# Optimization experiments

Hardware: AMD Instinct MI355X
Metric: run time of the kernel (lower is better)

## Reference

```python
import jax, jax.numpy as jnp
import numpy as np

ALPHA = 0.1      # LeakyReLU negative slope from GAT.__init__
NEG_INF = -9e15  # standard pyGAT masking constant


def gat_layer(x, adj, W, a_src, a_dst):
    """Single-head GraphAttentionLayer (n_heads=1, concat=True, dropout=0)."""
    Wh = x @ W                              # [N, F]
    f_src = Wh @ a_src                      # [N]
    f_dst = Wh @ a_dst                      # [N]
    e = jax.nn.leaky_relu(f_src[:, None] + f_dst[None, :], negative_slope=ALPHA)  # [N, N]
    e = jnp.where(adj > 0, e, NEG_INF)
    attn = jax.nn.softmax(e, axis=1)        # row-wise segment softmax over neighbors
    out = attn @ Wh                         # [N, F]
    return jax.nn.relu(out)                 # activate_function = 'relu'


def setup_inputs() -> dict:
    key = jax.random.key(0)
    ks = jax.random.split(key, 8)
    N, D_IN, D_HID, D_OUT = 8192, 256, 200, 128
    A_hat = (jax.random.uniform(ks[0], (N, N)) < 0.005).astype(jnp.float32)
    x = jax.random.normal(ks[1], (N, D_IN), dtype=jnp.float32)
    W1 = jax.random.normal(ks[2], (D_IN, D_HID), dtype=jnp.float32) * (1.0 / np.sqrt(D_IN))
    a1_src = jax.random.normal(ks[3], (D_HID,), dtype=jnp.float32) * 0.1
    a1_dst = jax.random.normal(ks[4], (D_HID,), dtype=jnp.float32) * 0.1
    W2 = jax.random.normal(ks[5], (D_HID, D_OUT), dtype=jnp.float32) * (1.0 / np.sqrt(D_HID))
    a2_src = jax.random.normal(ks[6], (D_OUT,), dtype=jnp.float32) * 0.1
    a2_dst = jax.random.normal(ks[7], (D_OUT,), dtype=jnp.float32) * 0.1
    return {"A_hat": A_hat, "x": x, "W1": W1, "a1_src": a1_src, "a1_dst": a1_dst,
            "W2": W2, "a2_src": a2_src, "a2_dst": a2_dst}


def reference(A_hat, x, W1, a1_src, a1_dst, W2, a2_src, a2_dst):
    # forward_direct with num_GCN_blocks = 2 (directed graph: A and A^T branches)
    A_t = A_hat.T
    params = [(W1, a1_src, a1_dst), (W2, a2_src, a2_dst)]
    outputs = [x]
    h1, h2 = x, x
    for (W, asrc, adst) in params:
        o1 = gat_layer(h1, A_hat, W, asrc, adst)
        o2 = gat_layer(h2, A_t, W, asrc, adst)
        outputs.append(jnp.concatenate([o1, o2], axis=1))
        h1, h2 = o1, o2
    return tuple(outputs)
```

## Files before the change

kernel.cpp:

```cpp
#include <hip/hip_runtime.h>
#include <hip/hip_bf16.h>

#define NN 8192
#define CAP 128
#define ALPHA 0.1f

typedef __attribute__((ext_vector_type(8))) short bf16x8;
typedef __attribute__((ext_vector_type(4))) float f32x4;
typedef __attribute__((ext_vector_type(4))) float nfloat4;

__global__ __launch_bounds__(256) void build_ell_rows(
        const float* __restrict__ A, int* __restrict__ deg,
        int* __restrict__ ell, int* __restrict__ degT,
        int* __restrict__ ellT) {
    __shared__ int cnt;
    __shared__ int idxs[CAP];
    const int i = blockIdx.x;
    const int tid = threadIdx.x;
    if (tid == 0) cnt = 0;
    __syncthreads();
    const nfloat4* rowA = (const nfloat4*)(A + (size_t)i * NN);
#pragma unroll
    for (int it = 0; it < NN / 4 / 256; ++it) {
        nfloat4 v = __builtin_nontemporal_load(&rowA[it * 256 + tid]);
        int j0 = (it * 256 + tid) * 4;
#pragma unroll
        for (int u = 0; u < 4; ++u) {
            if (v[u] > 0.f) {
                int p = atomicAdd(&cnt, 1);
                if (p < CAP) idxs[p] = j0 + u;
            }
        }
    }
    __syncthreads();
    int c = cnt;
    if (tid == 0) deg[i] = c;
    if (c > CAP) c = CAP;
    for (int t = tid; t < c; t += 256) {
        int j = idxs[t];
        ell[i * CAP + t] = j;
        int q = atomicAdd(&degT[j], 1);
        if (q < CAP) ellT[j * CAP + q] = i;
    }
}

__global__ void conv_bf16(const float* __restrict__ src,
                          __hip_bfloat16* __restrict__ dst, long long n) {
    long long i = ((long long)blockIdx.x * blockDim.x + threadIdx.x) * 4;
    if (i + 3 < n) {
        float4 v = *(const float4*)(src + i);
        dst[i + 0] = __float2bfloat16(v.x);
        dst[i + 1] = __float2bfloat16(v.y);
        dst[i + 2] = __float2bfloat16(v.z);
        dst[i + 3] = __float2bfloat16(v.w);
    } else {
        for (; i < n; ++i) dst[i] = __float2bfloat16(src[i]);
    }
}

__global__ void prep_wt(const float* __restrict__ W, int K, int N,
                        __hip_bfloat16* __restrict__ WT, int Kpad, int Npad) {
    int idx = blockIdx.x * blockDim.x + threadIdx.x;
    if (idx >= Npad * Kpad) return;
    int n = idx / Kpad, k = idx % Kpad;
    float v = (n < N && k < K) ? W[(size_t)k * N + n] : 0.f;
    WT[idx] = __float2bfloat16(v);
}

__global__ __launch_bounds__(256) void gemm_mfma(
        const __hip_bfloat16* __restrict__ Ab, int lda, long long aBatch,
        const __hip_bfloat16* __restrict__ BTb, int ldb,
        float* __restrict__ C, int ldc, long long cBatch,
        int Kpad, int Ncols) {
    __shared__ __hip_bfloat16 As[64 * 32];
    __shared__ __hip_bfloat16 Bs[64 * 32];
    const int tid = threadIdx.x;
    const int wave = tid >> 6, lane = tid & 63;
    const int bm = blockIdx.y * 64, bn = blockIdx.x * 64;
    const __hip_bfloat16* Abz = Ab + (size_t)blockIdx.z * aBatch;
    float* Cz = C + (size_t)blockIdx.z * cBatch;

    const int sr = tid >> 2, sc = tid & 3;
    const int kh_a = sc ^ ((sr >> 1) & 3);
    const __hip_bfloat16* gA = Abz + (size_t)(bm + sr) * lda + kh_a * 8;
    const __hip_bfloat16* gB = BTb + (size_t)(bn + sr) * ldb + kh_a * 8;
    char* ldsA = (char*)As + wave * 1024;
    char* ldsB = (char*)Bs + wave * 1024;

    const int fr = lane & 15;
    const int kh = lane >> 4;
    const int ar = wave * 16 + fr;
    const int aoff = ar * 64 + ((kh ^ ((ar >> 1) & 3)) * 16);
    int boff[4];
#pragma unroll
    for (int cb = 0; cb < 4; ++cb) {
        int bc = cb * 16 + fr;
        boff[cb] = bc * 64 + ((kh ^ ((bc >> 1) & 3)) * 16);
    }

    f32x4 acc[4] = {};
    for (int k0 = 0; k0 < Kpad; k0 += 32) {
        __builtin_amdgcn_global_load_lds(
            (const __attribute__((address_space(1))) void*)(gA + k0),
            (__attribute__((address_space(3))) void*)ldsA, 16, 0, 0);
        __builtin_amdgcn_global_load_lds(
            (const __attribute__((address_space(1))) void*)(gB + k0),
            (__attribute__((address_space(3))) void*)ldsB, 16, 0, 0);
        asm volatile("s_waitcnt vmcnt(0)" ::: "memory");
        __syncthreads();
        bf16x8 afrag = *(const bf16x8*)((const char*)As + aoff);
#pragma unroll
        for (int cb = 0; cb < 4; ++cb) {
            bf16x8 bfrag = *(const bf16x8*)((const char*)Bs + boff[cb]);
            acc[cb] = __builtin_amdgcn_mfma_f32_16x16x32_bf16(afrag, bfrag,
                                                              acc[cb], 0, 0, 0);
        }
        __syncthreads();
    }
    const int crow = bm + wave * 16 + (lane >> 4) * 4;
#pragma unroll
    for (int cb = 0; cb < 4; ++cb) {
        int col = bn + cb * 16 + (lane & 15);
        if (col < Ncols) {
#pragma unroll
            for (int r = 0; r < 4; ++r)
                Cz[(size_t)(crow + r) * ldc + col] = acc[cb][r];
        }
    }
}

__global__ void fvec_kernel(const float* __restrict__ Wh, int ldw, int F,
                            const float* __restrict__ asrc,
                            const float* __restrict__ adst,
                            float* __restrict__ fs, float* __restrict__ fd,
                            int M) {
    int wave = (int)((blockIdx.x * (long long)blockDim.x + threadIdx.x) >> 6);
    int lane = threadIdx.x & 63;
    if (wave >= M) return;
    const float* row = Wh + (long long)wave * ldw;
    float s = 0.f, d = 0.f;
    for (int k = lane; k < F; k += 64) {
        float w = row[k];
        s += w * asrc[k];
        d += w * adst[k];
    }
#pragma unroll
    for (int off = 32; off > 0; off >>= 1) {
        s += __shfl_down(s, off);
        d += __shfl_down(d, off);
    }
    if (lane == 0) { fs[wave] = s; fd[wave] = d; }
}

__global__ __launch_bounds__(128) void attn_kernel(
        const int* __restrict__ ell, const int* __restrict__ deg,
        const int* __restrict__ ellT, const int* __restrict__ degT,
        const float* __restrict__ fs, const float* __restrict__ fd,
        long long fStride,
        const float* __restrict__ Wh, long long whStride, int ldw, int F,
        float* __restrict__ out, int ldo,
        __hip_bfloat16* __restrict__ hb, long long hbStride, int ldh) {
    __shared__ float p[CAP];
    __shared__ int nbr[CAP];
    __shared__ float red[2];
    const int i = blockIdx.x;
    const int br = blockIdx.y;
    const int tid = threadIdx.x;
    const int* ep = br ? ellT : ell;
    const int* dp = br ? degT : deg;
    const float* fsp = fs + (size_t)br * fStride;
    const float* fdp = fd + (size_t)br * fStride;
    const float* Whp = Wh + (size_t)br * whStride;
    float* outp = out + br * F;
    __hip_bfloat16* hbp = hb ? hb + (size_t)br * hbStride : nullptr;

    int d = dp[i];
    if (d > CAP) d = CAP;

    if (d == 0) {
        for (int f = tid; f < F; f += blockDim.x) {
            float acc = 0.f;
            for (int j = 0; j < NN; ++j) acc += Whp[(long long)j * ldw + f];
            float v = acc / (float)NN;
            v = v > 0.f ? v : 0.f;
            outp[(long long)i * ldo + f] = v;
            if (hbp) hbp[(long long)i * ldh + f] = __float2bfloat16(v);
        }
        if (hbp)
            for (int f = F + tid; f < ldh; f += blockDim.x)
                hbp[(long long)i * ldh + f] = __float2bfloat16(0.f);
        return;
    }

    float fsi = fsp[i];
    if (tid < d) {
        int j = ep[i * CAP + tid];
        nbr[tid] = j;
        float e = fsi + fdp[j];
        p[tid] = e > 0.f ? e : ALPHA * e;
    }
    __syncthreads();
    if (tid < 64) {
        float m = -1e30f;
        for (int t = tid; t < d; t += 64) m = fmaxf(m, p[t]);
#pragma unroll
        for (int off = 32; off > 0; off >>= 1) m = fmaxf(m, __shfl_down(m, off));
        if (tid == 0) red[0] = m;
    }
    __syncthreads();
    float m = red[0];
    if (tid < d) p[tid] = __expf(p[tid] - m);
    __syncthreads();
    if (tid < 64) {
        float s = 0.f;
        for (int t = tid; t < d; t += 64) s += p[t];
#pragma unroll
        for (int off = 32; off > 0; off >>= 1) s += __shfl_down(s, off);
        if (tid == 0) red[1] = s;
    }
    __syncthreads();
    if (tid < d) p[tid] *= (1.f / red[1]);
    __syncthreads();

    const int fh = F >> 1;
    if (tid < fh) {
        float ax = 0.f, ay = 0.f;
        int t = 0;
        for (; t + 4 <= d; t += 4) {
            float2 w0 = ((const float2*)(Whp + (long long)nbr[t + 0] * ldw))[tid];
            float2 w1 = ((const float2*)(Whp + (long long)nbr[t + 1] * ldw))[tid];
            float2 w2 = ((const float2*)(Whp + (long long)nbr[t + 2] * ldw))[tid];
            float2 w3 = ((const float2*)(Whp + (long long)nbr[t + 3] * ldw))[tid];
            ax += p[t] * w0.x + p[t + 1] * w1.x + p[t + 2] * w2.x + p[t + 3] * w3.x;
            ay += p[t] * w0.y + p[t + 1] * w1.y + p[t + 2] * w2.y + p[t + 3] * w3.y;
        }
        for (; t < d; ++t) {
            float2 w = ((const float2*)(Whp + (long long)nbr[t] * ldw))[tid];
            ax += p[t] * w.x;
            ay += p[t] * w.y;
        }
        ax = ax > 0.f ? ax : 0.f;
        ay = ay > 0.f ? ay : 0.f;
        float2 v2 = {ax, ay};
        *(float2*)(outp + (long long)i * ldo + 2 * tid) = v2;
        if (hbp) {
            hbp[(long long)i * ldh + 2 * tid]     = __float2bfloat16(ax);
            hbp[(long long)i * ldh + 2 * tid + 1] = __float2bfloat16(ay);
        }
    } else if (hbp && 2 * tid < ldh) {
        hbp[(long long)i * ldh + 2 * tid]     = __float2bfloat16(0.f);
        hbp[(long long)i * ldh + 2 * tid + 1] = __float2bfloat16(0.f);
    }
}

static inline char* carve(char*& w, size_t bytes) {
    char* p = w;
    w += (bytes + 255) & ~(size_t)255;
    return p;
}

extern "C" void kernel_launch(void* const* d_in, const int* in_sizes, int n_in,
                              void* d_out, int out_size, void* d_ws,
                              size_t ws_size, hipStream_t stream) {
    const float* A   = (const float*)d_in[0];
    const float* x   = (const float*)d_in[1];
    const float* W1  = (const float*)d_in[2];
    const float* a1s = (const float*)d_in[3];
    const float* a1d = (const float*)d_in[4];
    const float* W2  = (const float*)d_in[5];
    const float* a2s = (const float*)d_in[6];
    const float* a2d = (const float*)d_in[7];
    float* out = (float*)d_out;

    const int D_IN = 256, D_HID = 200, D_OUT = 128;
    const int KP1 = 256;
    const int HP  = 224;
    const int NP1 = 256;

    char* w = (char*)d_ws;
    int* deg  = (int*)carve(w, NN * 4);
    int* degT = (int*)carve(w, NN * 4);
    int* ell  = (int*)carve(w, (size_t)NN * CAP * 4);
    int* ellT = (int*)carve(w, (size_t)NN * CAP * 4);
    float* Wh1 = (float*)carve(w, (size_t)NN * D_HID * 4);
    float* Wh2 = (float*)carve(w, (size_t)2 * NN * D_OUT * 4);
    float* fs1 = (float*)carve(w, NN * 4);
    float* fd1 = (float*)carve(w, NN * 4);
    float* fs2 = (float*)carve(w, (size_t)2 * NN * 4);
    float* fd2 = (float*)carve(w, (size_t)2 * NN * 4);
    __hip_bfloat16* xb   = (__hip_bfloat16*)carve(w, (size_t)NN * KP1 * 2);
    __hip_bfloat16* W1Tb = (__hip_bfloat16*)carve(w, (size_t)NP1 * KP1 * 2);
    __hip_bfloat16* W2Tb = (__hip_bfloat16*)carve(w, (size_t)D_OUT * HP * 2);
    __hip_bfloat16* h1b  = (__hip_bfloat16*)carve(w, (size_t)2 * NN * HP * 2);

    float* out0 = out;
    float* out1 = out + (size_t)NN * D_IN;
    float* out2 = out1 + (size_t)NN * 2 * D_HID;

    (void)hipMemsetAsync(degT, 0, NN * 4, stream);
    (void)hipMemcpyAsync(out0, x, (size_t)NN * D_IN * 4,
                         hipMemcpyDeviceToDevice, stream);

    conv_bf16<<<(NN * D_IN / 4 + 255) / 256, 256, 0, stream>>>(
        x, xb, (long long)NN * D_IN);
    prep_wt<<<(NP1 * KP1 + 255) / 256, 256, 0, stream>>>(W1, D_IN, D_HID,
                                                         W1Tb, KP1, NP1);
    prep_wt<<<(D_OUT * HP + 255) / 256, 256, 0, stream>>>(W2, D_HID, D_OUT,
                                                          W2Tb, HP, D_OUT);
    build_ell_rows<<<NN, 256, 0, stream>>>(A, deg, ell, degT, ellT);

    gemm_mfma<<<dim3(4, NN / 64, 1), 256, 0, stream>>>(
        xb, KP1, 0, W1Tb, KP1, Wh1, D_HID, 0, KP1, D_HID);
    fvec_kernel<<<NN / 4, 256, 0, stream>>>(Wh1, D_HID, D_HID, a1s, a1d, fs1,
                                            fd1, NN);
    attn_kernel<<<dim3(NN, 2), 128, 0, stream>>>(
        ell, deg, ellT, degT, fs1, fd1, 0, Wh1, 0, D_HID, D_HID,
        out1, 2 * D_HID, h1b, (long long)NN * HP, HP);

    gemm_mfma<<<dim3(2, NN / 64, 2), 256, 0, stream>>>(
        h1b, HP, (long long)NN * HP, W2Tb, HP, Wh2, D_OUT,
        (long long)NN * D_OUT, HP, D_OUT);
    fvec_kernel<<<2 * NN / 4, 256, 0, stream>>>(Wh2, D_OUT, D_OUT, a2s, a2d,
                                                fs2, fd2, 2 * NN);
    attn_kernel<<<dim3(NN, 2), 128, 0, stream>>>(
        ell, deg, ellT, degT, fs2, fd2, (long long)NN,
        Wh2, (long long)NN * D_OUT, D_OUT, D_OUT,
        out2, 2 * D_OUT, nullptr, 0, 0);
}
```

Before: 484.0 us.

## Fuse prep kernels, GEMM with attention-vector epilogue, and use single-wave attention

The code merges the x copy, bf16 conversions, weight transposes and buffer zeroing into one prep kernel, and runs the first GEMM and the ELL build in the same launch. The f_src/f_dst dot products move into the GEMM epilogue as atomic adds, which removes the separate fvec kernels. Attention now uses one 64-lane wave per row with float4 loads, shuffle-based softmax and no LDS barriers. The goal is fewer launches and less synchronisation overhead. In exchange, atomic accumulation makes the fs/fd summation order nondeterministic.

```diff
diff --git a/kernel.cpp b/kernel.cpp
--- a/kernel.cpp
+++ b/kernel.cpp
@@ -9,86 +9,66 @@
 typedef __attribute__((ext_vector_type(4))) float f32x4;
 typedef __attribute__((ext_vector_type(4))) float nfloat4;
 
-__global__ __launch_bounds__(256) void build_ell_rows(
-        const float* __restrict__ A, int* __restrict__ deg,
-        int* __restrict__ ell, int* __restrict__ degT,
-        int* __restrict__ ellT) {
-    __shared__ int cnt;
-    __shared__ int idxs[CAP];
-    const int i = blockIdx.x;
-    const int tid = threadIdx.x;
-    if (tid == 0) cnt = 0;
-    __syncthreads();
-    const nfloat4* rowA = (const nfloat4*)(A + (size_t)i * NN);
-#pragma unroll
-    for (int it = 0; it < NN / 4 / 256; ++it) {
-        nfloat4 v = __builtin_nontemporal_load(&rowA[it * 256 + tid]);
-        int j0 = (it * 256 + tid) * 4;
-#pragma unroll
-        for (int u = 0; u < 4; ++u) {
-            if (v[u] > 0.f) {
-                int p = atomicAdd(&cnt, 1);
-                if (p < CAP) idxs[p] = j0 + u;
-            }
-        }
-    }
-    __syncthreads();
-    int c = cnt;
-    if (tid == 0) deg[i] = c;
-    if (c > CAP) c = CAP;
-    for (int t = tid; t < c; t += 256) {
-        int j = idxs[t];
-        ell[i * CAP + t] = j;
-        int q = atomicAdd(&degT[j], 1);
-        if (q < CAP) ellT[j * CAP + q] = i;
-    }
-}
-
-__global__ void conv_bf16(const float* __restrict__ src,
-                          __hip_bfloat16* __restrict__ dst, long long n) {
-    long long i = ((long long)blockIdx.x * blockDim.x + threadIdx.x) * 4;
-    if (i + 3 < n) {
-        float4 v = *(const float4*)(src + i);
-        dst[i + 0] = __float2bfloat16(v.x);
-        dst[i + 1] = __float2bfloat16(v.y);
-        dst[i + 2] = __float2bfloat16(v.z);
-        dst[i + 3] = __float2bfloat16(v.w);
+static __device__ __forceinline__ unsigned short f2bf(float f) {
+    __hip_bfloat16 b = __float2bfloat16(f);
+    return *reinterpret_cast<unsigned short*>(&b);
+}
+
+__global__ __launch_bounds__(256) void prep_all(
+        const float* __restrict__ x, const float* __restrict__ W1,
+        const float* __restrict__ W2, __hip_bfloat16* __restrict__ xb,
+        __hip_bfloat16* __restrict__ W1Tb, __hip_bfloat16* __restrict__ W2Tb,
+        float* __restrict__ out0, int* __restrict__ degT,
+        float* __restrict__ fzero) {
+    const int b = blockIdx.x, tid = threadIdx.x;
+    if (b < 2048) {
+        long long i = ((long long)b * 256 + tid) * 4;
+        nfloat4 v = *(const nfloat4*)(x + i);
+        *(nfloat4*)(out0 + i) = v;
+        ushort4 h;
+        h.x = f2bf(v[0]); h.y = f2bf(v[1]); h.z = f2bf(v[2]); h.w = f2bf(v[3]);
+        *(ushort4*)(xb + i) = h;
+    } else if (b < 2104) {
+        int wb = b - 2048;
+        int w0 = wb * 1024 + tid * 4;
+        if (w0 < 8192) {
+            int4 z = {0, 0, 0, 0};
+            *(int4*)(degT + w0) = z;
+        } else {
+            nfloat4 z = {0.f, 0.f, 0.f, 0.f};
+            *(nfloat4*)(fzero + (w0 - 8192)) = z;
+        }
+    } else if (b < 2360) {
+        int idx = (b - 2104) * 256 + tid;
+        int n = idx >> 8, k = idx & 255;
+        W1Tb[idx] = __float2bfloat16(n < 200 ? W1[(size_t)k * 200 + n] : 0.f);
     } else {
-        for (; i < n; ++i) dst[i] = __float2bfloat16(src[i]);
-    }
-}
-
-__global__ void prep_wt(const float* __restrict__ W, int K, int N,
-                        __hip_bfloat16* __restrict__ WT, int Kpad, int Npad) {
-    int idx = blockIdx.x * blockDim.x + threadIdx.x;
-    if (idx >= Npad * Kpad) return;
-    int n = idx / Kpad, k = idx % Kpad;
-    float v = (n < N && k < K) ? W[(size_t)k * N + n] : 0.f;
-    WT[idx] = __float2bfloat16(v);
-}
-
-__global__ __launch_bounds__(256) void gemm_mfma(
-        const __hip_bfloat16* __restrict__ Ab, int lda, long long aBatch,
+        int idx = (b - 2360) * 256 + tid;
+        int n = idx / 224, k = idx % 224;
+        W2Tb[idx] = __float2bfloat16(k < 200 ? W2[(size_t)k * 128 + n] : 0.f);
+    }
+}
+
+__device__ __forceinline__ void gemm_body(
+        char* smem, int bm, int bn,
+        const __hip_bfloat16* __restrict__ Ab, int lda,
         const __hip_bfloat16* __restrict__ BTb, int ldb,
-        float* __restrict__ C, int ldc, long long cBatch,
-        int Kpad, int Ncols) {
-    __shared__ __hip_bfloat16 As[64 * 32];
-    __shared__ __hip_bfloat16 Bs[64 * 32];
+        float* __restrict__ C, int ldc, int Kpad, int Ncols,
+        const float* __restrict__ asrc, const float* __restrict__ adst,
+        float* __restrict__ fs, float* __restrict__ fd) {
+    __hip_bfloat16* As = (__hip_bfloat16*)smem;
+    __hip_bfloat16* Bs = (__hip_bfloat16*)(smem + 4096);
     const int tid = threadIdx.x;
     const int wave = tid >> 6, lane = tid & 63;
-    const int bm = blockIdx.y * 64, bn = blockIdx.x * 64;
-    const __hip_bfloat16* Abz = Ab + (size_t)blockIdx.z * aBatch;
-    float* Cz = C + (size_t)blockIdx.z * cBatch;
 
     const int sr = tid >> 2, sc = tid & 3;
     const int kh_a = sc ^ ((sr >> 1) & 3);
-    const __hip_bfloat16* gA = Abz + (size_t)(bm + sr) * lda + kh_a * 8;
+    const __hip_bfloat16* gA = Ab + (size_t)(bm + sr) * lda + kh_a * 8;
     const __hip_bfloat16* gB = BTb + (size_t)(bn + sr) * ldb + kh_a * 8;
     char* ldsA = (char*)As + wave * 1024;
     char* ldsB = (char*)Bs + wave * 1024;
 
-    const int fr = lane & 15;
-    const int kh = lane >> 4;
+    const int fr = lane & 15, kh = lane >> 4;
     const int ar = wave * 16 + fr;
     const int aoff = ar * 64 + ((kh ^ ((ar >> 1) & 3)) * 16);
     int boff[4];
@@ -117,139 +97,210 @@
         }
         __syncthreads();
     }
-    const int crow = bm + wave * 16 + (lane >> 4) * 4;
+
+    const int crow = bm + wave * 16 + kh * 4;
+    float as4[4], ad4[4];
+    int cols[4];
 #pragma unroll
     for (int cb = 0; cb < 4; ++cb) {
-        int col = bn + cb * 16 + (lane & 15);
+        int col = bn + cb * 16 + fr;
+        cols[cb] = col;
+        bool v = col < Ncols;
+        as4[cb] = v ? asrc[col] : 0.f;
+        ad4[cb] = v ? adst[col] : 0.f;
+    }
+#pragma unroll
+    for (int r = 0; r < 4; ++r) {
+        float s = 0.f, dd = 0.f;
+#pragma unroll
+        for (int cb = 0; cb < 4; ++cb) {
+            s += acc[cb][r] * as4[cb];
+            dd += acc[cb][r] * ad4[cb];
+        }
+#pragma unroll
+        for (int off = 8; off > 0; off >>= 1) {
+            s += __shfl_down(s, off, 16);
+            dd += __shfl_down(dd, off, 16);
+        }
+        if (fr == 0) {
+            atomicAdd(&fs[crow + r], s);
+            atomicAdd(&fd[crow + r], dd);
+        }
+    }
+#pragma unroll
+    for (int cb = 0; cb < 4; ++cb) {
+        int col = cols[cb];
         if (col < Ncols) {
 #pragma unroll
             for (int r = 0; r < 4; ++r)
-                Cz[(size_t)(crow + r) * ldc + col] = acc[cb][r];
-        }
-    }
-}
-
-__global__ void fvec_kernel(const float* __restrict__ Wh, int ldw, int F,
-                            const float* __restrict__ asrc,
-                            const float* __restrict__ adst,
-                            float* __restrict__ fs, float* __restrict__ fd,
-                            int M) {
-    int wave = (int)((blockIdx.x * (long long)blockDim.x + threadIdx.x) >> 6);
-    int lane = threadIdx.x & 63;
-    if (wave >= M) return;
-    const float* row = Wh + (long long)wave * ldw;
-    float s = 0.f, d = 0.f;
-    for (int k = lane; k < F; k += 64) {
-        float w = row[k];
-        s += w * asrc[k];
-        d += w * adst[k];
-    }
-#pragma unroll
-    for (int off = 32; off > 0; off >>= 1) {
-        s += __shfl_down(s, off);
-        d += __shfl_down(d, off);
-    }
-    if (lane == 0) { fs[wave] = s; fd[wave] = d; }
-}
-
-__global__ __launch_bounds__(128) void attn_kernel(
+                C[(size_t)(crow + r) * ldc + col] = acc[cb][r];
+        }
+    }
+}
+
+__global__ __launch_bounds__(256) void mega1(
+        const __hip_bfloat16* __restrict__ xb,
+        const __hip_bfloat16* __restrict__ W1Tb, float* __restrict__ Wh1,
+        const float* __restrict__ a1s, const float* __restrict__ a1d,
+        float* __restrict__ fs1, float* __restrict__ fd1,
+        const float* __restrict__ A, int* __restrict__ deg,
+        int* __restrict__ ell, int* __restrict__ degT,
+        int* __restrict__ ellT) {
+    __shared__ __align__(16) char smem[8192];
+    if (blockIdx.x < 512) {
+        gemm_body(smem, (int)(blockIdx.x >> 2) * 64, (int)(blockIdx.x & 3) * 64,
+                  xb, 256, W1Tb, 256, Wh1, 200, 256, 200, a1s, a1d, fs1, fd1);
+        return;
+    }
+    const int i = blockIdx.x - 512;
+    const int tid = threadIdx.x;
+    int* cnt = (int*)smem;
+    int* idxs = (int*)(smem + 16);
+    if (tid == 0) *cnt = 0;
+    __syncthreads();
+    const nfloat4* rowA = (const nfloat4*)(A + (size_t)i * NN);
+#pragma unroll
+    for (int it = 0; it < NN / 4 / 256; ++it) {
+        nfloat4 v = __builtin_nontemporal_load(&rowA[it * 256 + tid]);
+        int j0 = (it * 256 + tid) * 4;
+#pragma unroll
+        for (int u = 0; u < 4; ++u) {
+            if (v[u] > 0.f) {
+                int p = atomicAdd(cnt, 1);
+                if (p < CAP) idxs[p] = j0 + u;
+            }
+        }
+    }
+    __syncthreads();
+    int c = *cnt;
+    if (tid == 0) deg[i] = c;
+    if (c > CAP) c = CAP;
+    for (int t = tid; t < c; t += 256) {
+        int j = idxs[t];
+        ell[i * CAP + t] = j;
+        int q = atomicAdd(&degT[j], 1);
+        if (q < CAP) ellT[j * CAP + q] = i;
+    }
+}
+
+__global__ __launch_bounds__(256) void gemm2_kernel(
+        const __hip_bfloat16* __restrict__ h1b,
+        const __hip_bfloat16* __restrict__ W2Tb, float* __restrict__ Wh2,
+        const float* __restrict__ a2s, const float* __restrict__ a2d,
+        float* __restrict__ fs2, float* __restrict__ fd2) {
+    __shared__ __align__(16) char smem[8192];
+    const size_t z = blockIdx.z;
+    gemm_body(smem, (int)blockIdx.y * 64, (int)blockIdx.x * 64,
+              h1b + z * NN * 224, 224, W2Tb, 224, Wh2 + z * NN * 128, 128,
+              224, 128, a2s, a2d, fs2 + z * NN, fd2 + z * NN);
+}
+
+__global__ __launch_bounds__(64) void attn64(
         const int* __restrict__ ell, const int* __restrict__ deg,
         const int* __restrict__ ellT, const int* __restrict__ degT,
         const float* __restrict__ fs, const float* __restrict__ fd,
         long long fStride,
-        const float* __restrict__ Wh, long long whStride, int ldw, int F,
+        const float* __restrict__ Wh, long long whStride, int ldw, int F4,
         float* __restrict__ out, int ldo,
         __hip_bfloat16* __restrict__ hb, long long hbStride, int ldh) {
-    __shared__ float p[CAP];
-    __shared__ int nbr[CAP];
-    __shared__ float red[2];
-    const int i = blockIdx.x;
-    const int br = blockIdx.y;
-    const int tid = threadIdx.x;
+    const int i = blockIdx.x, br = blockIdx.y, lane = threadIdx.x;
     const int* ep = br ? ellT : ell;
     const int* dp = br ? degT : deg;
     const float* fsp = fs + (size_t)br * fStride;
     const float* fdp = fd + (size_t)br * fStride;
     const float* Whp = Wh + (size_t)br * whStride;
-    float* outp = out + br * F;
-    __hip_bfloat16* hbp = hb ? hb + (size_t)br * hbStride : nullptr;
+    const int F = F4 * 4;
+    float* outp = out + (size_t)i * ldo + br * F;
+    __hip_bfloat16* hbp = hb ? hb + (size_t)br * hbStride + (size_t)i * ldh
+                             : nullptr;
 
     int d = dp[i];
     if (d > CAP) d = CAP;
 
     if (d == 0) {
-        for (int f = tid; f < F; f += blockDim.x) {
+        for (int f = lane; f < F; f += 64) {
             float acc = 0.f;
-            for (int j = 0; j < NN; ++j) acc += Whp[(long long)j * ldw + f];
-            float v = acc / (float)NN;
-            v = v > 0.f ? v : 0.f;
-            outp[(long long)i * ldo + f] = v;
-            if (hbp) hbp[(long long)i * ldh + f] = __float2bfloat16(v);
+            for (int j = 0; j < NN; ++j) acc += Whp[(size_t)j * ldw + f];
+            float v = fmaxf(acc / (float)NN, 0.f);
+            outp[f] = v;
+            if (hbp) hbp[f] = __float2bfloat16(v);
         }
         if (hbp)
-            for (int f = F + tid; f < ldh; f += blockDim.x)
-                hbp[(long long)i * ldh + f] = __float2bfloat16(0.f);
+            for (int f = F + lane; f < ldh; f += 64)
+                hbp[f] = __float2bfloat16(0.f);
         return;
     }
 
-    float fsi = fsp[i];
-    if (tid < d) {
-        int j = ep[i * CAP + tid];
-        nbr[tid] = j;
-        float e = fsi + fdp[j];
-        p[tid] = e > 0.f ? e : ALPHA * e;
-    }
-    __syncthreads();
-    if (tid < 64) {
-        float m = -1e30f;
-        for (int t = tid; t < d; t += 64) m = fmaxf(m, p[t]);
-#pragma unroll
-        for (int off = 32; off > 0; off >>= 1) m = fmaxf(m, __shfl_down(m, off));
-        if (tid == 0) red[0] = m;
-    }
-    __syncthreads();
-    float m = red[0];
-    if (tid < d) p[tid] = __expf(p[tid] - m);
-    __syncthreads();
-    if (tid < 64) {
-        float s = 0.f;
-        for (int t = tid; t < d; t += 64) s += p[t];
-#pragma unroll
-        for (int off = 32; off > 0; off >>= 1) s += __shfl_down(s, off);
-        if (tid == 0) red[1] = s;
-    }
-    __syncthreads();
-    if (tid < d) p[tid] *= (1.f / red[1]);
-    __syncthreads();
-
-    const int fh = F >> 1;
-    if (tid < fh) {
-        float ax = 0.f, ay = 0.f;
-        int t = 0;
-        for (; t + 4 <= d; t += 4) {
-            float2 w0 = ((const float2*)(Whp + (long long)nbr[t + 0] * ldw))[tid];
-            float2 w1 = ((const float2*)(Whp + (long long)nbr[t + 1] * ldw))[tid];
-            float2 w2 = ((const float2*)(Whp + (long long)nbr[t + 2] * ldw))[tid];
-            float2 w3 = ((const float2*)(Whp + (long long)nbr[t + 3] * ldw))[tid];
-            ax += p[t] * w0.x + p[t + 1] * w1.x + p[t + 2] * w2.x + p[t + 3] * w3.x;
-            ay += p[t] * w0.y + p[t + 1] * w1.y + p[t + 2] * w2.y + p[t + 3] * w3.y;
-        }
-        for (; t < d; ++t) {
-            float2 w = ((const float2*)(Whp + (long long)nbr[t] * ldw))[tid];
-            ax += p[t] * w.x;
-            ay += p[t] * w.y;
-        }
-        ax = ax > 0.f ? ax : 0.f;
-        ay = ay > 0.f ? ay : 0.f;
-        float2 v2 = {ax, ay};
-        *(float2*)(outp + (long long)i * ldo + 2 * tid) = v2;
+    const float fsi = fsp[i];
+    int n0 = 0, n1 = 0;
+    float e0 = -1e30f, e1 = -1e30f;
+    if (lane < d) {
+        n0 = ep[i * CAP + lane];
+        float e = fsi + fdp[n0];
+        e0 = e > 0.f ? e : ALPHA * e;
+    }
+    if (lane + 64 < d) {
+        n1 = ep[i * CAP + lane + 64];
+        float e = fsi + fdp[n1];
+        e1 = e > 0.f ? e : ALPHA * e;
+    }
+    float m = fmaxf(e0, e1);
+#pragma unroll
+    for (int off = 32; off > 0; off >>= 1) m = fmaxf(m, __shfl_xor(m, off));
+    float p0 = (lane < d) ? __expf(e0 - m) : 0.f;
+    float p1 = (lane + 64 < d) ? __expf(e1 - m) : 0.f;
+    float s = p0 + p1;
+#pragma unroll
+    for (int off = 32; off > 0; off >>= 1) s += __shfl_xor(s, off);
+    const float inv = 1.f / s;
+    p0 *= inv;
+    p1 *= inv;
+
+    const nfloat4* base = (const nfloat4*)Whp;
+    const int ld4 = ldw >> 2;
+    const bool act = lane < F4;
+    nfloat4 acc = {0.f, 0.f, 0.f, 0.f};
+
+    const int dc = d < 64 ? d : 64;
+    int t = 0;
+    for (; t + 4 <= dc; t += 4) {
+        int j0 = __shfl(n0, t), j1 = __shfl(n0, t + 1);
+        int j2 = __shfl(n0, t + 2), j3 = __shfl(n0, t + 3);
+        float a0 = __shfl(p0, t), a1 = __shfl(p0, t + 1);
+        float a2 = __shfl(p0, t + 2), a3 = __shfl(p0, t + 3);
+        if (act) {
+            nfloat4 w0 = base[(size_t)j0 * ld4 + lane];
+            nfloat4 w1 = base[(size_t)j1 * ld4 + lane];
+            nfloat4 w2 = base[(size_t)j2 * ld4 + lane];
+            nfloat4 w3 = base[(size_t)j3 * ld4 + lane];
+            acc += a0 * w0 + a1 * w1 + a2 * w2 + a3 * w3;
+        }
+    }
+    for (; t < dc; ++t) {
+        int j = __shfl(n0, t);
+        float a = __shfl(p0, t);
+        if (act) acc += a * base[(size_t)j * ld4 + lane];
+    }
+    for (t = 64; t < d; ++t) {
+        int j = __shfl(n1, t - 64);
+        float a = __shfl(p1, t - 64);
+        if (act) acc += a * base[(size_t)j * ld4 + lane];
+    }
+
+    if (act) {
+        nfloat4 v;
+        v[0] = fmaxf(acc[0], 0.f); v[1] = fmaxf(acc[1], 0.f);
+        v[2] = fmaxf(acc[2], 0.f); v[3] = fmaxf(acc[3], 0.f);
+        *(nfloat4*)(outp + 4 * lane) = v;
         if (hbp) {
-            hbp[(long long)i * ldh + 2 * tid]     = __float2bfloat16(ax);
-            hbp[(long long)i * ldh + 2 * tid + 1] = __float2bfloat16(ay);
-        }
-    } else if (hbp && 2 * tid < ldh) {
-        hbp[(long long)i * ldh + 2 * tid]     = __float2bfloat16(0.f);
-        hbp[(long long)i * ldh + 2 * tid + 1] = __float2bfloat16(0.f);
+            ushort4 h;
+            h.x = f2bf(v[0]); h.y = f2bf(v[1]);
+            h.z = f2bf(v[2]); h.w = f2bf(v[3]);
+            *(ushort4*)(hbp + 4 * lane) = h;
+        }
+    } else if (hbp && 4 * lane < ldh) {
+        ushort4 z = {0, 0, 0, 0};
+        *(ushort4*)(hbp + 4 * lane) = z;
     }
 }
 
@@ -273,9 +324,7 @@
     float* out = (float*)d_out;
 
     const int D_IN = 256, D_HID = 200, D_OUT = 128;
-    const int KP1 = 256;
-    const int HP  = 224;
-    const int NP1 = 256;
+    const int HP = 224;
 
     char* w = (char*)d_ws;
     int* deg  = (int*)carve(w, NN * 4);
@@ -284,46 +333,35 @@
     int* ellT = (int*)carve(w, (size_t)NN * CAP * 4);
     float* Wh1 = (float*)carve(w, (size_t)NN * D_HID * 4);
     float* Wh2 = (float*)carve(w, (size_t)2 * NN * D_OUT * 4);
-    float* fs1 = (float*)carve(w, NN * 4);
-    float* fd1 = (float*)carve(w, NN * 4);
-    float* fs2 = (float*)carve(w, (size_t)2 * NN * 4);
-    float* fd2 = (float*)carve(w, (size_t)2 * NN * 4);
-    __hip_bfloat16* xb   = (__hip_bfloat16*)carve(w, (size_t)NN * KP1 * 2);
-    __hip_bfloat16* W1Tb = (__hip_bfloat16*)carve(w, (size_t)NP1 * KP1 * 2);
-    __hip_bfloat16* W2Tb = (__hip_bfloat16*)carve(w, (size_t)D_OUT * HP * 2);
+    float* fzero = (float*)carve(w, (size_t)49152 * 4);
+    float* fs1 = fzero;
+    float* fd1 = fzero + 8192;
+    float* fs2 = fzero + 16384;
+    float* fd2 = fzero + 32768;
+    __hip_bfloat16* xb   = (__hip_bfloat16*)carve(w, (size_t)NN * 256 * 2);
+    __hip_bfloat16* W1Tb = (__hip_bfloat16*)carve(w, (size_t)256 * 256 * 2);
+    __hip_bfloat16* W2Tb = (__hip_bfloat16*)carve(w, (size_t)128 * HP * 2);
     __hip_bfloat16* h1b  = (__hip_bfloat16*)carve(w, (size_t)2 * NN * HP * 2);
 
     float* out0 = out;
     float* out1 = out + (size_t)NN * D_IN;
     float* out2 = out1 + (size_t)NN * 2 * D_HID;
 
-    (void)hipMemsetAsync(degT, 0, NN * 4, stream);
-    (void)hipMemcpyAsync(out0, x, (size_t)NN * D_IN * 4,
-                         hipMemcpyDeviceToDevice, stream);
-
-    conv_bf16<<<(NN * D_IN / 4 + 255) / 256, 256, 0, stream>>>(
-        x, xb, (long long)NN * D_IN);
-    prep_wt<<<(NP1 * KP1 + 255) / 256, 256, 0, stream>>>(W1, D_IN, D_HID,
-                                                         W1Tb, KP1, NP1);
-    prep_wt<<<(D_OUT * HP + 255) / 256, 256, 0, stream>>>(W2, D_HID, D_OUT,
-                                                          W2Tb, HP, D_OUT);
-    build_ell_rows<<<NN, 256, 0, stream>>>(A, deg, ell, degT, ellT);
-
-    gemm_mfma<<<dim3(4, NN / 64, 1), 256, 0, stream>>>(
-        xb, KP1, 0, W1Tb, KP1, Wh1, D_HID, 0, KP1, D_HID);
-    fvec_kernel<<<NN / 4, 256, 0, stream>>>(Wh1, D_HID, D_HID, a1s, a1d, fs1,
-                                            fd1, NN);
-    attn_kernel<<<dim3(NN, 2), 128, 0, stream>>>(
-        ell, deg, ellT, degT, fs1, fd1, 0, Wh1, 0, D_HID, D_HID,
+    prep_all<<<2472, 256, 0, stream>>>(x, W1, W2, xb, W1Tb, W2Tb, out0, degT,
+                                       fzero);
+
+    mega1<<<512 + NN, 256, 0, stream>>>(xb, W1Tb, Wh1, a1s, a1d, fs1, fd1, A,
+                                        deg, ell, degT, ellT);
+
+    attn64<<<dim3(NN, 2), 64, 0, stream>>>(
+        ell, deg, ellT, degT, fs1, fd1, 0, Wh1, 0, D_HID, D_HID / 4,
         out1, 2 * D_HID, h1b, (long long)NN * HP, HP);
 
-    gemm_mfma<<<dim3(2, NN / 64, 2), 256, 0, stream>>>(
-        h1b, HP, (long long)NN * HP, W2Tb, HP, Wh2, D_OUT,
-        (long long)NN * D_OUT, HP, D_OUT);
-    fvec_kernel<<<2 * NN / 4, 256, 0, stream>>>(Wh2, D_OUT, D_OUT, a2s, a2d,
-                                                fs2, fd2, 2 * NN);
-    attn_kernel<<<dim3(NN, 2), 128, 0, stream>>>(
-        ell, deg, ellT, degT, fs2, fd2, (long long)NN,
-        Wh2, (long long)NN * D_OUT, D_OUT, D_OUT,
+    gemm2_kernel<<<dim3(2, NN / 64, 2), 256, 0, stream>>>(h1b, W2Tb, Wh2, a2s,
+                                                          a2d, fs2, fd2);
+
+    attn64<<<dim3(NN, 2), 64, 0, stream>>>(
+        ell, deg, ellT, degT, fs2, fd2, (long long)NN, Wh2,
+        (long long)NN * D_OUT, D_OUT, D_OUT / 4,
         out2, 2 * D_OUT, nullptr, 0, 0);
 }
```

New measurement: 448.3 us. 1.08x faster.
